# Kernel optimization log

Hardware: AMD Instinct MI355X
Metric: run time of the kernel (lower is better)

The kernel has to match this reference:

```python
import jax, jax.numpy as jnp
import numpy as np

N, E, H, R = 20000, 400000, 128, 20


def setup_inputs() -> dict:
    key = jax.random.key(0)
    ks = jax.random.split(key, 12)
    inv_h = 1.0 / np.sqrt(H)
    inv_r = 1.0 / np.sqrt(R)
    return {
        "s": jax.random.normal(ks[0], (N, H), jnp.float32),
        "v": jax.random.normal(ks[1], (N, 3, H), jnp.float32),
        "edge_rbf": jax.random.normal(ks[2], (E, R), jnp.float32),
        "edge_cutoff": jax.random.uniform(ks[3], (E,), jnp.float32),
        "edge_vec": jax.random.normal(ks[4], (E, 3), jnp.float32),
        "W1": jax.random.normal(ks[5], (H, H), jnp.float32) * inv_h,
        "b1": jnp.zeros((H,), jnp.float32),
        "W2": jax.random.normal(ks[6], (H, 3 * H), jnp.float32) * inv_h,
        "b2": jnp.zeros((3 * H,), jnp.float32),
        "Wr": jax.random.normal(ks[7], (R, 3 * H), jnp.float32) * inv_r,
        "br": jnp.zeros((3 * H,), jnp.float32),
        "edge_index": jax.random.randint(ks[8], (2, E), 0, N, jnp.int64),
    }


def reference(s, v, edge_rbf, edge_cutoff, edge_vec, W1, b1, W2, b2, Wr, br, edge_index):
    i, j = edge_index[0], edge_index[1]
    n = s.shape[0]
    # rbf projection modulated by cutoff: [E, 3H]
    W = (edge_rbf @ Wr + br) * edge_cutoff[:, None]
    # scalar MLP on gathered source features: [E, 3H]
    h = jax.nn.silu(s[j] @ W1 + b1)
    x = (h @ W2 + b2) * W
    x_ss, x_sv, x_vv = jnp.split(x, 3, axis=-1)  # each [E, H]
    ds = jax.ops.segment_sum(x_ss, i, num_segments=n)
    # dv1: outer product of edge direction with gated scalars -> [E,3,H]
    dv1 = jax.ops.segment_sum(x_sv[:, None, :] * edge_vec[:, :, None], i, num_segments=n)
    # equivariant term: project v_j onto edge direction, re-expand
    inner = jnp.sum(v[j] * edge_vec[:, :, None], axis=1)  # [E, H]
    dv2 = jax.ops.segment_sum((inner * x_vv)[:, None, :] * edge_vec[:, :, None], i, num_segments=n)
    return ds, dv1 + dv2
```

## Files before the change

### kernel.cpp

```cpp
#include <hip/hip_runtime.h>
#include <hip/hip_bf16.h>

#define HDIM 128
#define H3   384
#define RDIM 20
#define NPB  16
#define EPB  64

typedef unsigned short u16;
typedef unsigned int   u32;

__device__ __forceinline__ u16 f2bf(float f) {
    __hip_bfloat16 h = __float2bfloat16(f);
    return *(u16*)&h;
}
__device__ __forceinline__ float bflo(u32 u) {
    union { u32 i; float f; } x; x.i = u << 16; return x.f;
}
__device__ __forceinline__ float bfhi(u32 u) {
    union { u32 i; float f; } x; x.i = u & 0xffff0000u; return x.f;
}
__device__ __forceinline__ u32 pk(float lo, float hi) {
    return (u32)f2bf(lo) | ((u32)f2bf(hi) << 16);
}

__global__ __launch_bounds__(128) void node_mlp_kernel(
    const float* __restrict__ s, const float* __restrict__ W1,
    const float* __restrict__ b1, const float* __restrict__ W2,
    const float* __restrict__ b2, const float* __restrict__ v,
    u32* __restrict__ P3, int N)
{
    __shared__ float sS[NPB][HDIM];
    __shared__ float sH[NPB][HDIM];
    const int t  = threadIdx.x;
    const int n0 = blockIdx.x * NPB;

    #pragma unroll
    for (int n = 0; n < NPB; ++n) {
        int node = n0 + n;
        sS[n][t] = (node < N) ? s[(size_t)node * HDIM + t] : 0.f;
    }
    __syncthreads();

    float acc[NPB];
    #pragma unroll
    for (int n = 0; n < NPB; ++n) acc[n] = 0.f;
    for (int k = 0; k < HDIM; ++k) {
        float w = W1[k * HDIM + t];
        #pragma unroll
        for (int n = 0; n < NPB; ++n) acc[n] += sS[n][k] * w;
    }
    float bb = b1[t];
    #pragma unroll
    for (int n = 0; n < NPB; ++n) {
        float z = acc[n] + bb;
        sH[n][t] = z / (1.f + __expf(-z));
    }
    __syncthreads();

    float a0[NPB], a1[NPB], a2[NPB];
    #pragma unroll
    for (int n = 0; n < NPB; ++n) { a0[n] = 0.f; a1[n] = 0.f; a2[n] = 0.f; }
    for (int k2 = 0; k2 < HDIM / 2; ++k2) {
        float2 hv[NPB];
        #pragma unroll
        for (int n = 0; n < NPB; ++n) hv[n] = ((const float2*)sH[n])[k2];
        #pragma unroll
        for (int kk = 0; kk < 2; ++kk) {
            int k = 2 * k2 + kk;
            float w0 = W2[k * H3 + t];
            float w1 = W2[k * H3 + t + 128];
            float w2 = W2[k * H3 + t + 256];
            #pragma unroll
            for (int n = 0; n < NPB; ++n) {
                float h = kk ? hv[n].y : hv[n].x;
                a0[n] += h * w0;
                a1[n] += h * w1;
                a2[n] += h * w2;
            }
        }
    }
    float c0 = b2[t], c1 = b2[t + 128], c2 = b2[t + 256];
    #pragma unroll
    for (int n = 0; n < NPB; ++n) {
        int node = n0 + n;
        if (node < N) {
            size_t vb = (size_t)node * H3;
            float vx = v[vb + t], vy = v[vb + 128 + t], vz = v[vb + 256 + t];
            size_t pb = (size_t)node * H3 + t;
            P3[pb]       = pk(a0[n] + c0, a1[n] + c1);
            P3[pb + 128] = pk(a2[n] + c2, vx);
            P3[pb + 256] = pk(vy, vz);
        }
    }
}

__global__ void hist_kernel(const int* __restrict__ eidx, int* __restrict__ counts, int E)
{
    int e = blockIdx.x * 256 + threadIdx.x;
    if (e < E) atomicAdd(&counts[eidx[e]], 1);
}

__global__ __launch_bounds__(1024) void scan_kernel(
    const int* __restrict__ counts, int* __restrict__ rstart,
    int* __restrict__ cursor, int N)
{
    __shared__ int part[1024];
    const int t = threadIdx.x;
    const int C = 20;
    int loc[C];
    int s = 0;
    #pragma unroll
    for (int q = 0; q < C; ++q) {
        int idx = t * C + q;
        int c = (idx < N) ? counts[idx] : 0;
        loc[q] = s; s += c;
    }
    part[t] = s;
    __syncthreads();
    for (int off = 1; off < 1024; off <<= 1) {
        int vv = (t >= off) ? part[t - off] : 0;
        __syncthreads();
        part[t] += vv;
        __syncthreads();
    }
    int boff = (t > 0) ? part[t - 1] : 0;
    #pragma unroll
    for (int q = 0; q < C; ++q) {
        int idx = t * C + q;
        if (idx < N) {
            int st = boff + loc[q];
            rstart[idx] = st;
            cursor[idx] = st;
        }
    }
    if (t == 1023) rstart[N] = part[1023];
}

__global__ void scatter_kernel(const int* __restrict__ eidx, int* __restrict__ cursor,
                               int* __restrict__ eord, int E)
{
    int e = blockIdx.x * 256 + threadIdx.x;
    if (e < E) {
        int i = eidx[e];
        int pos = atomicAdd(&cursor[i], 1);
        eord[pos] = e;
    }
}

__global__ __launch_bounds__(128, 4) void edge_stream_kernel(
    const int* __restrict__ eord, const int* __restrict__ eidx,
    const float* __restrict__ rbf, const float* __restrict__ cutoff,
    const float* __restrict__ evec, const float* __restrict__ Wr,
    const float* __restrict__ br, const u32* __restrict__ P3,
    float* __restrict__ ds, float* __restrict__ dv, int E)
{
    const int t    = threadIdx.x;
    const int base = blockIdx.x * EPB;
    const int cnt  = min(EPB, E - base);

    float wr[3 * RDIM];
    #pragma unroll
    for (int k = 0; k < RDIM; ++k) {
        wr[k]            = Wr[k * H3 + t];
        wr[RDIM + k]     = Wr[k * H3 + t + 128];
        wr[2 * RDIM + k] = Wr[k * H3 + t + 256];
    }
    float br0 = br[t], br1 = br[t + 128], br2 = br[t + 256];
    #pragma unroll
    for (int k = 0; k < 3 * RDIM; ++k) asm volatile("" : "+v"(wr[k]));
    asm volatile("" : "+v"(br0), "+v"(br1), "+v"(br2));

    __shared__ int   sI[EPB], sJ[EPB];
    __shared__ float sCut[EPB], sVx[EPB], sVy[EPB], sVz[EPB];
    __shared__ __attribute__((aligned(16))) float sRbf[EPB][RDIM];

    if (t < cnt) {
        int e   = eord[base + t];
        sI[t]   = eidx[e];
        sJ[t]   = eidx[E + e] * H3;
        sCut[t] = cutoff[e];
        sVx[t]  = evec[3 * e];
        sVy[t]  = evec[3 * e + 1];
        sVz[t]  = evec[3 * e + 2];
        const float4* rr = (const float4*)(rbf + (size_t)e * RDIM);
        float4* dst = (float4*)sRbf[t];
        #pragma unroll
        for (int j = 0; j < 5; ++j) dst[j] = rr[j];
    }
    __syncthreads();

    u32 ca, cb, cc;
    {
        int idx = sJ[0] + t;
        ca = P3[idx]; cb = P3[idx + 128]; cc = P3[idx + 256];
    }
    int   cur  = sI[0];
    float accs = 0.f, accx = 0.f, accy = 0.f, accz = 0.f;

    for (int q = 0; q < cnt; ++q) {
        u32 na = 0, nb = 0, nc = 0;
        if (q + 1 < cnt) {
            int idx = sJ[q + 1] + t;
            na = P3[idx]; nb = P3[idx + 128]; nc = P3[idx + 256];
        }
        int iq = sI[q];
        if (iq != cur) {
            atomicAdd(&ds[(size_t)cur * HDIM + t], accs);
            size_t dvi = (size_t)cur * H3;
            atomicAdd(&dv[dvi + t],       accx);
            atomicAdd(&dv[dvi + 128 + t], accy);
            atomicAdd(&dv[dvi + 256 + t], accz);
            accs = accx = accy = accz = 0.f;
            cur = iq;
        }
        const float4* r4 = (const float4*)sRbf[q];
        float w0 = 0.f, w1 = 0.f, w2 = 0.f;
        #pragma unroll
        for (int k4 = 0; k4 < 5; ++k4) {
            float4 r = r4[k4];
            w0 += r.x * wr[4*k4]          + r.y * wr[4*k4+1]          + r.z * wr[4*k4+2]          + r.w * wr[4*k4+3];
            w1 += r.x * wr[RDIM+4*k4]     + r.y * wr[RDIM+4*k4+1]     + r.z * wr[RDIM+4*k4+2]     + r.w * wr[RDIM+4*k4+3];
            w2 += r.x * wr[2*RDIM+4*k4]   + r.y * wr[2*RDIM+4*k4+1]   + r.z * wr[2*RDIM+4*k4+2]   + r.w * wr[2*RDIM+4*k4+3];
        }
        float cu = sCut[q];
        float ex = sVx[q], ey = sVy[q], ez = sVz[q];
        float pss = bflo(ca), psv = bfhi(ca);
        float pvv = bflo(cb), vx  = bfhi(cb);
        float vy  = bflo(cc), vz  = bfhi(cc);
        float xss = (w0 + br0) * cu * pss;
        float xsv = (w1 + br1) * cu * psv;
        float xvv = (w2 + br2) * cu * pvv;
        float inner = vx * ex + vy * ey + vz * ez;
        float coef  = xsv + inner * xvv;
        accs += xss;
        accx += coef * ex;
        accy += coef * ey;
        accz += coef * ez;
        ca = na; cb = nb; cc = nc;
    }
    atomicAdd(&ds[(size_t)cur * HDIM + t], accs);
    size_t dvi = (size_t)cur * H3;
    atomicAdd(&dv[dvi + t],       accx);
    atomicAdd(&dv[dvi + 128 + t], accy);
    atomicAdd(&dv[dvi + 256 + t], accz);
}

extern "C" void kernel_launch(void* const* d_in, const int* in_sizes, int n_in,
                              void* d_out, int out_size, void* d_ws, size_t ws_size,
                              hipStream_t stream)
{
    const float* s    = (const float*)d_in[0];
    const float* v    = (const float*)d_in[1];
    const float* rbf  = (const float*)d_in[2];
    const float* cut  = (const float*)d_in[3];
    const float* evec = (const float*)d_in[4];
    const float* W1   = (const float*)d_in[5];
    const float* b1   = (const float*)d_in[6];
    const float* W2   = (const float*)d_in[7];
    const float* b2   = (const float*)d_in[8];
    const float* Wr   = (const float*)d_in[9];
    const float* br   = (const float*)d_in[10];
    const int*   eidx = (const int*)d_in[11];

    const int N = in_sizes[0] / HDIM;
    const int E = in_sizes[3];

    float* out = (float*)d_out;
    float* ds  = out;
    float* dv  = out + (size_t)N * HDIM;

    char* w = (char*)d_ws;
    u32* P3 = (u32*)w;                     w += ((size_t)N * H3 * 4 + 255) / 256 * 256;
    int* counts = (int*)w;                 w += ((size_t)N * 4 + 255) / 256 * 256;
    int* rstart = (int*)w;                 w += ((size_t)(N + 1) * 4 + 255) / 256 * 256;
    int* cursor = (int*)w;                 w += ((size_t)N * 4 + 255) / 256 * 256;
    int* eord   = (int*)w;

    hipMemsetAsync(d_out, 0, (size_t)out_size * sizeof(float), stream);
    hipMemsetAsync(counts, 0, (size_t)N * sizeof(int), stream);

    node_mlp_kernel<<<(N + NPB - 1) / NPB, 128, 0, stream>>>(s, W1, b1, W2, b2, v, P3, N);
    hist_kernel<<<(E + 255) / 256, 256, 0, stream>>>(eidx, counts, E);
    scan_kernel<<<1, 1024, 0, stream>>>(counts, rstart, cursor, N);
    scatter_kernel<<<(E + 255) / 256, 256, 0, stream>>>(eidx, cursor, eord, E);
    edge_stream_kernel<<<(E + EPB - 1) / EPB, 128, 0, stream>>>(eord, eidx, rbf, cut,
                                                                evec, Wr, br, P3,
                                                                ds, dv, E);
}
```

Before: 318.6 us.

## Split edge kernel into three warp-role groups per output component

The edge streaming kernel now runs 384 threads per block, split into three 128-thread roles that handle the ss, sv and vv channels separately, each with its own 20-weight register slice. Per-thread register pressure drops from 60 weights and 4 accumulators. The rbf rows are no longer staged in shared memory; each role streams them straight from global memory with a one-edge-ahead prefetch. Edges per block double to 128. In exchange, each rbf row is read three times and dv gets two atomic contributions per element (roles 1 and 2) instead of one, which raises atomic traffic.

```diff
diff --git a/kernel.cpp b/kernel.cpp
--- a/kernel.cpp
+++ b/kernel.cpp
@@ -5,7 +5,8 @@
 #define H3   384
 #define RDIM 20
 #define NPB  16
-#define EPB  64
+#define EPB  128
+#define TPB  384
 
 typedef unsigned short u16;
 typedef unsigned int   u32;
@@ -148,7 +149,18 @@
     }
 }
 
-__global__ __launch_bounds__(128, 4) void edge_stream_kernel(
+#define LOAD_ROW(dst, q) {                                           \
+    const float4* rp = (const float4*)(rbf + (size_t)sE[q] * RDIM);  \
+    dst[0]=rp[0]; dst[1]=rp[1]; dst[2]=rp[2]; dst[3]=rp[3]; dst[4]=rp[4]; }
+
+#define DOT20(res, rr) {                                                         \
+    res = brv;                                                                   \
+    _Pragma("unroll")                                                            \
+    for (int k4 = 0; k4 < 5; ++k4)                                               \
+        res += rr[k4].x*wr[4*k4] + rr[k4].y*wr[4*k4+1] +                         \
+               rr[k4].z*wr[4*k4+2] + rr[k4].w*wr[4*k4+3]; }
+
+__global__ __launch_bounds__(TPB) void edge_stream_kernel(
     const int* __restrict__ eord, const int* __restrict__ eidx,
     const float* __restrict__ rbf, const float* __restrict__ cutoff,
     const float* __restrict__ evec, const float* __restrict__ Wr,
@@ -156,94 +168,126 @@
     float* __restrict__ ds, float* __restrict__ dv, int E)
 {
     const int t    = threadIdx.x;
+    const int ch   = t & (HDIM - 1);
+    const int role = t >> 7;
     const int base = blockIdx.x * EPB;
     const int cnt  = min(EPB, E - base);
 
-    float wr[3 * RDIM];
-    #pragma unroll
-    for (int k = 0; k < RDIM; ++k) {
-        wr[k]            = Wr[k * H3 + t];
-        wr[RDIM + k]     = Wr[k * H3 + t + 128];
-        wr[2 * RDIM + k] = Wr[k * H3 + t + 256];
-    }
-    float br0 = br[t], br1 = br[t + 128], br2 = br[t + 256];
-    #pragma unroll
-    for (int k = 0; k < 3 * RDIM; ++k) asm volatile("" : "+v"(wr[k]));
-    asm volatile("" : "+v"(br0), "+v"(br1), "+v"(br2));
-
-    __shared__ int   sI[EPB], sJ[EPB];
+    float wr[RDIM];
+    #pragma unroll
+    for (int k = 0; k < RDIM; ++k) wr[k] = Wr[k * H3 + role * HDIM + ch];
+    const float brv = br[role * HDIM + ch];
+
+    __shared__ int   sE[EPB], sI[EPB], sJ[EPB];
     __shared__ float sCut[EPB], sVx[EPB], sVy[EPB], sVz[EPB];
-    __shared__ __attribute__((aligned(16))) float sRbf[EPB][RDIM];
 
     if (t < cnt) {
         int e   = eord[base + t];
+        sE[t]   = e;
         sI[t]   = eidx[e];
         sJ[t]   = eidx[E + e] * H3;
         sCut[t] = cutoff[e];
         sVx[t]  = evec[3 * e];
         sVy[t]  = evec[3 * e + 1];
         sVz[t]  = evec[3 * e + 2];
-        const float4* rr = (const float4*)(rbf + (size_t)e * RDIM);
-        float4* dst = (float4*)sRbf[t];
-        #pragma unroll
-        for (int j = 0; j < 5; ++j) dst[j] = rr[j];
     }
     __syncthreads();
 
-    u32 ca, cb, cc;
-    {
-        int idx = sJ[0] + t;
-        ca = P3[idx]; cb = P3[idx + 128]; cc = P3[idx + 256];
-    }
-    int   cur  = sI[0];
-    float accs = 0.f, accx = 0.f, accy = 0.f, accz = 0.f;
-
-    for (int q = 0; q < cnt; ++q) {
-        u32 na = 0, nb = 0, nc = 0;
-        if (q + 1 < cnt) {
-            int idx = sJ[q + 1] + t;
-            na = P3[idx]; nb = P3[idx + 128]; nc = P3[idx + 256];
-        }
-        int iq = sI[q];
-        if (iq != cur) {
-            atomicAdd(&ds[(size_t)cur * HDIM + t], accs);
-            size_t dvi = (size_t)cur * H3;
-            atomicAdd(&dv[dvi + t],       accx);
-            atomicAdd(&dv[dvi + 128 + t], accy);
-            atomicAdd(&dv[dvi + 256 + t], accz);
-            accs = accx = accy = accz = 0.f;
-            cur = iq;
-        }
-        const float4* r4 = (const float4*)sRbf[q];
-        float w0 = 0.f, w1 = 0.f, w2 = 0.f;
-        #pragma unroll
-        for (int k4 = 0; k4 < 5; ++k4) {
-            float4 r = r4[k4];
-            w0 += r.x * wr[4*k4]          + r.y * wr[4*k4+1]          + r.z * wr[4*k4+2]          + r.w * wr[4*k4+3];
-            w1 += r.x * wr[RDIM+4*k4]     + r.y * wr[RDIM+4*k4+1]     + r.z * wr[RDIM+4*k4+2]     + r.w * wr[RDIM+4*k4+3];
-            w2 += r.x * wr[2*RDIM+4*k4]   + r.y * wr[2*RDIM+4*k4+1]   + r.z * wr[2*RDIM+4*k4+2]   + r.w * wr[2*RDIM+4*k4+3];
-        }
-        float cu = sCut[q];
-        float ex = sVx[q], ey = sVy[q], ez = sVz[q];
-        float pss = bflo(ca), psv = bfhi(ca);
-        float pvv = bflo(cb), vx  = bfhi(cb);
-        float vy  = bflo(cc), vz  = bfhi(cc);
-        float xss = (w0 + br0) * cu * pss;
-        float xsv = (w1 + br1) * cu * psv;
-        float xvv = (w2 + br2) * cu * pvv;
-        float inner = vx * ex + vy * ey + vz * ez;
-        float coef  = xsv + inner * xvv;
-        accs += xss;
-        accx += coef * ex;
-        accy += coef * ey;
-        accz += coef * ez;
-        ca = na; cb = nb; cc = nc;
-    }
-    atomicAdd(&ds[(size_t)cur * HDIM + t], accs);
-    size_t dvi = (size_t)cur * H3;
-    atomicAdd(&dv[dvi + t],       accx);
-    atomicAdd(&dv[dvi + 128 + t], accy);
-    atomicAdd(&dv[dvi + 256 + t], accz);
+    int cur = sI[0];
+
+    if (role == 0) {
+        float4 rc[5], rn[5];
+        LOAD_ROW(rc, 0);
+        #pragma unroll
+        for (int j = 0; j < 5; ++j) rn[j] = rc[j];
+        u32 ca = P3[sJ[0] + ch];
+        float accs = 0.f;
+        for (int q = 0; q < cnt; ++q) {
+            int qn = q + 1;
+            u32 na = 0;
+            if (qn < cnt) { LOAD_ROW(rn, qn); na = P3[sJ[qn] + ch]; }
+            if (sI[q] != cur) {
+                atomicAdd(&ds[(size_t)cur * HDIM + ch], accs);
+                accs = 0.f; cur = sI[q];
+            }
+            float w; DOT20(w, rc);
+            accs += w * sCut[q] * bflo(ca);
+            #pragma unroll
+            for (int j = 0; j < 5; ++j) rc[j] = rn[j];
+            ca = na;
+        }
+        atomicAdd(&ds[(size_t)cur * HDIM + ch], accs);
+    } else if (role == 1) {
+        float4 rc[5], rn[5];
+        LOAD_ROW(rc, 0);
+        #pragma unroll
+        for (int j = 0; j < 5; ++j) rn[j] = rc[j];
+        u32 ca = P3[sJ[0] + ch];
+        float ax = 0.f, ay = 0.f, az = 0.f;
+        for (int q = 0; q < cnt; ++q) {
+            int qn = q + 1;
+            u32 na = 0;
+            if (qn < cnt) { LOAD_ROW(rn, qn); na = P3[sJ[qn] + ch]; }
+            if (sI[q] != cur) {
+                size_t dvi = (size_t)cur * H3;
+                atomicAdd(&dv[dvi + ch],       ax);
+                atomicAdd(&dv[dvi + 128 + ch], ay);
+                atomicAdd(&dv[dvi + 256 + ch], az);
+                ax = ay = az = 0.f; cur = sI[q];
+            }
+            float w; DOT20(w, rc);
+            float xsv = w * sCut[q] * bfhi(ca);
+            ax += xsv * sVx[q];
+            ay += xsv * sVy[q];
+            az += xsv * sVz[q];
+            #pragma unroll
+            for (int j = 0; j < 5; ++j) rc[j] = rn[j];
+            ca = na;
+        }
+        size_t dvi = (size_t)cur * H3;
+        atomicAdd(&dv[dvi + ch],       ax);
+        atomicAdd(&dv[dvi + 128 + ch], ay);
+        atomicAdd(&dv[dvi + 256 + ch], az);
+    } else {
+        float4 rc[5], rn[5];
+        LOAD_ROW(rc, 0);
+        #pragma unroll
+        for (int j = 0; j < 5; ++j) rn[j] = rc[j];
+        u32 cb = P3[sJ[0] + 128 + ch];
+        u32 cc = P3[sJ[0] + 256 + ch];
+        float ax = 0.f, ay = 0.f, az = 0.f;
+        for (int q = 0; q < cnt; ++q) {
+            int qn = q + 1;
+            u32 nb = 0, nc = 0;
+            if (qn < cnt) {
+                LOAD_ROW(rn, qn);
+                nb = P3[sJ[qn] + 128 + ch];
+                nc = P3[sJ[qn] + 256 + ch];
+            }
+            if (sI[q] != cur) {
+                size_t dvi = (size_t)cur * H3;
+                atomicAdd(&dv[dvi + ch],       ax);
+                atomicAdd(&dv[dvi + 128 + ch], ay);
+                atomicAdd(&dv[dvi + 256 + ch], az);
+                ax = ay = az = 0.f; cur = sI[q];
+            }
+            float w; DOT20(w, rc);
+            float ex = sVx[q], ey = sVy[q], ez = sVz[q];
+            float xvv   = w * sCut[q] * bflo(cb);
+            float inner = bfhi(cb) * ex + bflo(cc) * ey + bfhi(cc) * ez;
+            float tt    = inner * xvv;
+            ax += tt * ex;
+            ay += tt * ey;
+            az += tt * ez;
+            #pragma unroll
+            for (int j = 0; j < 5; ++j) rc[j] = rn[j];
+            cb = nb; cc = nc;
+        }
+        size_t dvi = (size_t)cur * H3;
+        atomicAdd(&dv[dvi + ch],       ax);
+        atomicAdd(&dv[dvi + 128 + ch], ay);
+        atomicAdd(&dv[dvi + 256 + ch], az);
+    }
 }
 
 extern "C" void kernel_launch(void* const* d_in, const int* in_sizes, int n_in,
@@ -284,7 +328,7 @@
     hist_kernel<<<(E + 255) / 256, 256, 0, stream>>>(eidx, counts, E);
     scan_kernel<<<1, 1024, 0, stream>>>(counts, rstart, cursor, N);
     scatter_kernel<<<(E + 255) / 256, 256, 0, stream>>>(eidx, cursor, eord, E);
-    edge_stream_kernel<<<(E + EPB - 1) / EPB, 128, 0, stream>>>(eord, eidx, rbf, cut,
+    edge_stream_kernel<<<(E + EPB - 1) / EPB, TPB, 0, stream>>>(eord, eidx, rbf, cut,
                                                                 evec, Wr, br, P3,
                                                                 ds, dv, E);
 }
```

Measured after the change: 495.2 us. +55.4%, slower.

## Precompute edge RBF projection with MFMA into bf16 workspace before edge pass

Applied to the files above, without the earlier changes.

Adds a separate kernel that computes the per-edge RBF projection (rbf @ Wr + br) * cutoff with bf16 MFMA instructions and writes it as a bf16 [E,384] buffer in sorted edge order. The edge streaming kernel then reads these precomputed weights instead of doing the 20-wide dot products per edge in FP32 registers, and it processes 128 edges per block. The aim is to move the FP32 ALU work onto matrix cores and free registers for occupancy. In exchange it adds about 300 MB of extra global write and read traffic plus bf16 rounding of the weights, and it keeps the old kernel as a fallback when the workspace is too small.

```diff
diff --git a/kernel.cpp b/kernel.cpp
--- a/kernel.cpp
+++ b/kernel.cpp
@@ -5,14 +5,19 @@
 #define H3   384
 #define RDIM 20
 #define NPB  16
-#define EPB  64
+#define EPB  128
 
 typedef unsigned short u16;
 typedef unsigned int   u32;
+typedef __attribute__((ext_vector_type(8))) short short8v;
+typedef __attribute__((ext_vector_type(4))) float f32x4;
 
 __device__ __forceinline__ u16 f2bf(float f) {
     __hip_bfloat16 h = __float2bfloat16(f);
     return *(u16*)&h;
+}
+__device__ __forceinline__ float bf2f(u16 u) {
+    union { u32 i; float f; } x; x.i = (u32)u << 16; return x.f;
 }
 __device__ __forceinline__ float bflo(u32 u) {
     union { u32 i; float f; } x; x.i = u << 16; return x.f;
@@ -148,7 +153,159 @@
     }
 }
 
-__global__ __launch_bounds__(128, 4) void edge_stream_kernel(
+__global__ __launch_bounds__(256) void wgemm_kernel(
+    const int* __restrict__ eord, const float* __restrict__ rbf,
+    const float* __restrict__ cutoff, const float* __restrict__ Wr,
+    const float* __restrict__ br, u16* __restrict__ Ws, int E)
+{
+    const int lane    = threadIdx.x & 63;
+    const int wave    = threadIdx.x >> 6;
+    const int g       = lane >> 4;
+    const int m       = lane & 15;
+    const int colhalf = wave & 1;
+    const int wgrp    = wave >> 1;
+
+    short8v bfrag[12];
+    float   brt[12];
+    #pragma unroll
+    for (int n = 0; n < 12; ++n) {
+        int col = colhalf * 192 + n * 16 + m;
+        short8v f;
+        #pragma unroll
+        for (int j = 0; j < 8; ++j) {
+            int k = 8 * g + j;
+            f[j] = (k < RDIM) ? (short)f2bf(Wr[k * H3 + col]) : (short)0;
+        }
+        bfrag[n] = f;
+        brt[n] = br[col];
+    }
+
+    const int PBI = 256;
+    for (int it = 0; it < PBI / 32; ++it) {
+        int pbase = blockIdx.x * PBI + it * 32 + wgrp * 16;
+        if (pbase >= E) break;
+
+        short8v af;
+        int posA = pbase + m;
+        if (posA < E && g < 3) {
+            const float* rr = rbf + (size_t)eord[posA] * RDIM;
+            if (g < 2) {
+                float4 r0 = *(const float4*)(rr + 8 * g);
+                float4 r1 = *(const float4*)(rr + 8 * g + 4);
+                af[0] = (short)f2bf(r0.x); af[1] = (short)f2bf(r0.y);
+                af[2] = (short)f2bf(r0.z); af[3] = (short)f2bf(r0.w);
+                af[4] = (short)f2bf(r1.x); af[5] = (short)f2bf(r1.y);
+                af[6] = (short)f2bf(r1.z); af[7] = (short)f2bf(r1.w);
+            } else {
+                float4 r0 = *(const float4*)(rr + 16);
+                af[0] = (short)f2bf(r0.x); af[1] = (short)f2bf(r0.y);
+                af[2] = (short)f2bf(r0.z); af[3] = (short)f2bf(r0.w);
+                af[4] = 0; af[5] = 0; af[6] = 0; af[7] = 0;
+            }
+        } else {
+            #pragma unroll
+            for (int j = 0; j < 8; ++j) af[j] = 0;
+        }
+
+        float cut[4];
+        #pragma unroll
+        for (int r = 0; r < 4; ++r) {
+            int pos = pbase + 4 * g + r;
+            cut[r] = (pos < E) ? cutoff[eord[pos]] : 0.f;
+        }
+
+        #pragma unroll
+        for (int n = 0; n < 12; ++n) {
+            f32x4 c = {0.f, 0.f, 0.f, 0.f};
+            c = __builtin_amdgcn_mfma_f32_16x16x32_bf16(af, bfrag[n], c, 0, 0, 0);
+            int col = colhalf * 192 + n * 16 + m;
+            #pragma unroll
+            for (int r = 0; r < 4; ++r) {
+                int pos = pbase + 4 * g + r;
+                if (pos < E)
+                    Ws[(size_t)pos * H3 + col] = f2bf((c[r] + brt[n]) * cut[r]);
+            }
+        }
+    }
+}
+
+__global__ __launch_bounds__(128) void edge_kernel(
+    const int* __restrict__ eord, const int* __restrict__ eidx,
+    const float* __restrict__ evec, const u16* __restrict__ Ws,
+    const u32* __restrict__ P3, float* __restrict__ ds,
+    float* __restrict__ dv, int E)
+{
+    const int t    = threadIdx.x;
+    const int base = blockIdx.x * EPB;
+    const int cnt  = min(EPB, E - base);
+
+    __shared__ int   sI[EPB], sJ[EPB];
+    __shared__ float sVx[EPB], sVy[EPB], sVz[EPB];
+
+    if (t < cnt) {
+        int e  = eord[base + t];
+        sI[t]  = eidx[e];
+        sJ[t]  = eidx[E + e] * H3;
+        sVx[t] = evec[3 * e];
+        sVy[t] = evec[3 * e + 1];
+        sVz[t] = evec[3 * e + 2];
+    }
+    __syncthreads();
+
+    const u16* wp = Ws + (size_t)base * H3 + t;
+
+    int   cur  = sI[0];
+    float accs = 0.f, accx = 0.f, accy = 0.f, accz = 0.f;
+
+    u32 ca, cb, cc; u16 w0c, w1c, w2c;
+    {
+        int idx = sJ[0] + t;
+        ca = P3[idx]; cb = P3[idx + 128]; cc = P3[idx + 256];
+        w0c = wp[0]; w1c = wp[128]; w2c = wp[256];
+    }
+
+    for (int q = 0; q < cnt; ++q) {
+        u32 na = 0, nb = 0, nc = 0; u16 w0n = 0, w1n = 0, w2n = 0;
+        if (q + 1 < cnt) {
+            int idx = sJ[q + 1] + t;
+            na = P3[idx]; nb = P3[idx + 128]; nc = P3[idx + 256];
+            const u16* wq = wp + (size_t)(q + 1) * H3;
+            w0n = wq[0]; w1n = wq[128]; w2n = wq[256];
+        }
+        if (sI[q] != cur) {
+            atomicAdd(&ds[(size_t)cur * HDIM + t], accs);
+            size_t dvi = (size_t)cur * H3;
+            atomicAdd(&dv[dvi + t],       accx);
+            atomicAdd(&dv[dvi + 128 + t], accy);
+            atomicAdd(&dv[dvi + 256 + t], accz);
+            accs = accx = accy = accz = 0.f;
+            cur = sI[q];
+        }
+        float w0 = bf2f(w0c), w1 = bf2f(w1c), w2 = bf2f(w2c);
+        float ex = sVx[q], ey = sVy[q], ez = sVz[q];
+        float pss = bflo(ca), psv = bfhi(ca);
+        float pvv = bflo(cb), vx  = bfhi(cb);
+        float vy  = bflo(cc), vz  = bfhi(cc);
+        float xss = w0 * pss;
+        float xsv = w1 * psv;
+        float xvv = w2 * pvv;
+        float inner = vx * ex + vy * ey + vz * ez;
+        float coef  = xsv + inner * xvv;
+        accs += xss;
+        accx += coef * ex;
+        accy += coef * ey;
+        accz += coef * ez;
+        ca = na; cb = nb; cc = nc;
+        w0c = w0n; w1c = w1n; w2c = w2n;
+    }
+    atomicAdd(&ds[(size_t)cur * HDIM + t], accs);
+    size_t dvi = (size_t)cur * H3;
+    atomicAdd(&dv[dvi + t],       accx);
+    atomicAdd(&dv[dvi + 128 + t], accy);
+    atomicAdd(&dv[dvi + 256 + t], accz);
+}
+
+__global__ __launch_bounds__(128, 4) void edge_stream_fallback(
     const int* __restrict__ eord, const int* __restrict__ eidx,
     const float* __restrict__ rbf, const float* __restrict__ cutoff,
     const float* __restrict__ evec, const float* __restrict__ Wr,
@@ -156,8 +313,8 @@
     float* __restrict__ ds, float* __restrict__ dv, int E)
 {
     const int t    = threadIdx.x;
-    const int base = blockIdx.x * EPB;
-    const int cnt  = min(EPB, E - base);
+    const int base = blockIdx.x * 64;
+    const int cnt  = min(64, E - base);
 
     float wr[3 * RDIM];
     #pragma unroll
@@ -166,14 +323,11 @@
         wr[RDIM + k]     = Wr[k * H3 + t + 128];
         wr[2 * RDIM + k] = Wr[k * H3 + t + 256];
     }
-    float br0 = br[t], br1 = br[t + 128], br2 = br[t + 256];
-    #pragma unroll
-    for (int k = 0; k < 3 * RDIM; ++k) asm volatile("" : "+v"(wr[k]));
-    asm volatile("" : "+v"(br0), "+v"(br1), "+v"(br2));
-
-    __shared__ int   sI[EPB], sJ[EPB];
-    __shared__ float sCut[EPB], sVx[EPB], sVy[EPB], sVz[EPB];
-    __shared__ __attribute__((aligned(16))) float sRbf[EPB][RDIM];
+    const float br0 = br[t], br1 = br[t + 128], br2 = br[t + 256];
+
+    __shared__ int   sI[64], sJ[64];
+    __shared__ float sCut[64], sVx[64], sVy[64], sVz[64];
+    __shared__ __attribute__((aligned(16))) float sRbf[64][RDIM];
 
     if (t < cnt) {
         int e   = eord[base + t];
@@ -204,24 +358,23 @@
             int idx = sJ[q + 1] + t;
             na = P3[idx]; nb = P3[idx + 128]; nc = P3[idx + 256];
         }
-        int iq = sI[q];
-        if (iq != cur) {
+        if (sI[q] != cur) {
             atomicAdd(&ds[(size_t)cur * HDIM + t], accs);
             size_t dvi = (size_t)cur * H3;
             atomicAdd(&dv[dvi + t],       accx);
             atomicAdd(&dv[dvi + 128 + t], accy);
             atomicAdd(&dv[dvi + 256 + t], accz);
             accs = accx = accy = accz = 0.f;
-            cur = iq;
+            cur = sI[q];
         }
         const float4* r4 = (const float4*)sRbf[q];
         float w0 = 0.f, w1 = 0.f, w2 = 0.f;
         #pragma unroll
         for (int k4 = 0; k4 < 5; ++k4) {
             float4 r = r4[k4];
-            w0 += r.x * wr[4*k4]          + r.y * wr[4*k4+1]          + r.z * wr[4*k4+2]          + r.w * wr[4*k4+3];
-            w1 += r.x * wr[RDIM+4*k4]     + r.y * wr[RDIM+4*k4+1]     + r.z * wr[RDIM+4*k4+2]     + r.w * wr[RDIM+4*k4+3];
-            w2 += r.x * wr[2*RDIM+4*k4]   + r.y * wr[2*RDIM+4*k4+1]   + r.z * wr[2*RDIM+4*k4+2]   + r.w * wr[2*RDIM+4*k4+3];
+            w0 += r.x*wr[4*k4]        + r.y*wr[4*k4+1]        + r.z*wr[4*k4+2]        + r.w*wr[4*k4+3];
+            w1 += r.x*wr[RDIM+4*k4]   + r.y*wr[RDIM+4*k4+1]   + r.z*wr[RDIM+4*k4+2]   + r.w*wr[RDIM+4*k4+3];
+            w2 += r.x*wr[2*RDIM+4*k4] + r.y*wr[2*RDIM+4*k4+1] + r.z*wr[2*RDIM+4*k4+2] + r.w*wr[2*RDIM+4*k4+3];
         }
         float cu = sCut[q];
         float ex = sVx[q], ey = sVy[q], ez = sVz[q];
@@ -270,12 +423,15 @@
     float* ds  = out;
     float* dv  = out + (size_t)N * HDIM;
 
-    char* w = (char*)d_ws;
+    char* w0 = (char*)d_ws;
+    char* w  = w0;
     u32* P3 = (u32*)w;                     w += ((size_t)N * H3 * 4 + 255) / 256 * 256;
     int* counts = (int*)w;                 w += ((size_t)N * 4 + 255) / 256 * 256;
     int* rstart = (int*)w;                 w += ((size_t)(N + 1) * 4 + 255) / 256 * 256;
     int* cursor = (int*)w;                 w += ((size_t)N * 4 + 255) / 256 * 256;
-    int* eord   = (int*)w;
+    int* eord   = (int*)w;                 w += ((size_t)E * 4 + 255) / 256 * 256;
+    u16* Ws     = (u16*)w;                 w += (size_t)E * H3 * 2;
+    bool haveWs = ((size_t)(w - w0) <= ws_size);
 
     hipMemsetAsync(d_out, 0, (size_t)out_size * sizeof(float), stream);
     hipMemsetAsync(counts, 0, (size_t)N * sizeof(int), stream);
@@ -284,7 +440,14 @@
     hist_kernel<<<(E + 255) / 256, 256, 0, stream>>>(eidx, counts, E);
     scan_kernel<<<1, 1024, 0, stream>>>(counts, rstart, cursor, N);
     scatter_kernel<<<(E + 255) / 256, 256, 0, stream>>>(eidx, cursor, eord, E);
-    edge_stream_kernel<<<(E + EPB - 1) / EPB, 128, 0, stream>>>(eord, eidx, rbf, cut,
+
+    if (haveWs) {
+        wgemm_kernel<<<(E + 255) / 256, 256, 0, stream>>>(eord, rbf, cut, Wr, br, Ws, E);
+        edge_kernel<<<(E + EPB - 1) / EPB, 128, 0, stream>>>(eord, eidx, evec, Ws, P3,
+                                                             ds, dv, E);
+    } else {
+        edge_stream_fallback<<<(E + 63) / 64, 128, 0, stream>>>(eord, eidx, rbf, cut,
                                                                 evec, Wr, br, P3,
                                                                 ds, dv, E);
-}
+    }
+}
```

Measured after the change: 319.8 us. Within noise of the previous version (+0.4%).

## Batch edge gathers in groups of eight and stream Wr from cache

Applied to the files above, without the earlier changes.

The edge loop now processes edges in groups of 8. It first issues all 24 packed-feature gathers for the group, then computes the rbf projection for all 8 edges together, reloading Wr rows from global memory (cache) instead of pinning 60 weights in registers. The aim is more memory-level parallelism than the previous one-edge-ahead prefetch, while keeping register pressure bounded by dropping the launch-bounds occupancy hint. The cost is repeated Wr loads per group and possibly lower occupancy, since the occupancy constraint was removed.

```diff
diff --git a/kernel.cpp b/kernel.cpp
--- a/kernel.cpp
+++ b/kernel.cpp
@@ -6,6 +6,7 @@
 #define RDIM 20
 #define NPB  16
 #define EPB  64
+#define GRP  8
 
 typedef unsigned short u16;
 typedef unsigned int   u32;
@@ -148,7 +149,7 @@
     }
 }
 
-__global__ __launch_bounds__(128, 4) void edge_stream_kernel(
+__global__ __launch_bounds__(128) void edge_stream_kernel(
     const int* __restrict__ eord, const int* __restrict__ eidx,
     const float* __restrict__ rbf, const float* __restrict__ cutoff,
     const float* __restrict__ evec, const float* __restrict__ Wr,
@@ -159,17 +160,8 @@
     const int base = blockIdx.x * EPB;
     const int cnt  = min(EPB, E - base);
 
-    float wr[3 * RDIM];
-    #pragma unroll
-    for (int k = 0; k < RDIM; ++k) {
-        wr[k]            = Wr[k * H3 + t];
-        wr[RDIM + k]     = Wr[k * H3 + t + 128];
-        wr[2 * RDIM + k] = Wr[k * H3 + t + 256];
-    }
-    float br0 = br[t], br1 = br[t + 128], br2 = br[t + 256];
-    #pragma unroll
-    for (int k = 0; k < 3 * RDIM; ++k) asm volatile("" : "+v"(wr[k]));
-    asm volatile("" : "+v"(br0), "+v"(br1), "+v"(br2));
+    const float* wp = Wr + t;
+    const float br0 = br[t], br1 = br[t + 128], br2 = br[t + 256];
 
     __shared__ int   sI[EPB], sJ[EPB];
     __shared__ float sCut[EPB], sVx[EPB], sVy[EPB], sVz[EPB];
@@ -190,54 +182,64 @@
     }
     __syncthreads();
 
-    u32 ca, cb, cc;
-    {
-        int idx = sJ[0] + t;
-        ca = P3[idx]; cb = P3[idx + 128]; cc = P3[idx + 256];
-    }
     int   cur  = sI[0];
     float accs = 0.f, accx = 0.f, accy = 0.f, accz = 0.f;
 
-    for (int q = 0; q < cnt; ++q) {
-        u32 na = 0, nb = 0, nc = 0;
-        if (q + 1 < cnt) {
-            int idx = sJ[q + 1] + t;
-            na = P3[idx]; nb = P3[idx + 128]; nc = P3[idx + 256];
-        }
-        int iq = sI[q];
-        if (iq != cur) {
-            atomicAdd(&ds[(size_t)cur * HDIM + t], accs);
-            size_t dvi = (size_t)cur * H3;
-            atomicAdd(&dv[dvi + t],       accx);
-            atomicAdd(&dv[dvi + 128 + t], accy);
-            atomicAdd(&dv[dvi + 256 + t], accz);
-            accs = accx = accy = accz = 0.f;
-            cur = iq;
-        }
-        const float4* r4 = (const float4*)sRbf[q];
-        float w0 = 0.f, w1 = 0.f, w2 = 0.f;
-        #pragma unroll
-        for (int k4 = 0; k4 < 5; ++k4) {
-            float4 r = r4[k4];
-            w0 += r.x * wr[4*k4]          + r.y * wr[4*k4+1]          + r.z * wr[4*k4+2]          + r.w * wr[4*k4+3];
-            w1 += r.x * wr[RDIM+4*k4]     + r.y * wr[RDIM+4*k4+1]     + r.z * wr[RDIM+4*k4+2]     + r.w * wr[RDIM+4*k4+3];
-            w2 += r.x * wr[2*RDIM+4*k4]   + r.y * wr[2*RDIM+4*k4+1]   + r.z * wr[2*RDIM+4*k4+2]   + r.w * wr[2*RDIM+4*k4+3];
-        }
-        float cu = sCut[q];
-        float ex = sVx[q], ey = sVy[q], ez = sVz[q];
-        float pss = bflo(ca), psv = bfhi(ca);
-        float pvv = bflo(cb), vx  = bfhi(cb);
-        float vy  = bflo(cc), vz  = bfhi(cc);
-        float xss = (w0 + br0) * cu * pss;
-        float xsv = (w1 + br1) * cu * psv;
-        float xvv = (w2 + br2) * cu * pvv;
-        float inner = vx * ex + vy * ey + vz * ez;
-        float coef  = xsv + inner * xvv;
-        accs += xss;
-        accx += coef * ex;
-        accy += coef * ey;
-        accz += coef * ez;
-        ca = na; cb = nb; cc = nc;
+    for (int g0 = 0; g0 < cnt; g0 += GRP) {
+        u32 pa[GRP], pb[GRP], pc[GRP];
+        #pragma unroll
+        for (int e = 0; e < GRP; ++e) {
+            int q = g0 + e;
+            int idx = sJ[(q < cnt) ? q : (cnt - 1)] + t;
+            pa[e] = P3[idx]; pb[e] = P3[idx + 128]; pc[e] = P3[idx + 256];
+        }
+
+        float d0[GRP], d1[GRP], d2[GRP];
+        #pragma unroll
+        for (int e = 0; e < GRP; ++e) { d0[e] = br0; d1[e] = br1; d2[e] = br2; }
+        #pragma unroll 4
+        for (int k = 0; k < RDIM; ++k) {
+            float w0 = wp[k * H3];
+            float w1 = wp[k * H3 + 128];
+            float w2 = wp[k * H3 + 256];
+            #pragma unroll
+            for (int e = 0; e < GRP; ++e) {
+                float r = sRbf[g0 + e][k];
+                d0[e] += r * w0;
+                d1[e] += r * w1;
+                d2[e] += r * w2;
+            }
+        }
+
+        #pragma unroll
+        for (int e = 0; e < GRP; ++e) {
+            int q = g0 + e;
+            if (q < cnt) {
+                if (sI[q] != cur) {
+                    atomicAdd(&ds[(size_t)cur * HDIM + t], accs);
+                    size_t dvi = (size_t)cur * H3;
+                    atomicAdd(&dv[dvi + t],       accx);
+                    atomicAdd(&dv[dvi + 128 + t], accy);
+                    atomicAdd(&dv[dvi + 256 + t], accz);
+                    accs = accx = accy = accz = 0.f;
+                    cur = sI[q];
+                }
+                float cu = sCut[q];
+                float ex = sVx[q], ey = sVy[q], ez = sVz[q];
+                float pss = bflo(pa[e]), psv = bfhi(pa[e]);
+                float pvv = bflo(pb[e]), vx  = bfhi(pb[e]);
+                float vy  = bflo(pc[e]), vz  = bfhi(pc[e]);
+                float xss = d0[e] * cu * pss;
+                float xsv = d1[e] * cu * psv;
+                float xvv = d2[e] * cu * pvv;
+                float inner = vx * ex + vy * ey + vz * ez;
+                float coef  = xsv + inner * xvv;
+                accs += xss;
+                accx += coef * ex;
+                accy += coef * ey;
+                accz += coef * ez;
+            }
+        }
     }
     atomicAdd(&ds[(size_t)cur * HDIM + t], accs);
     size_t dvi = (size_t)cur * H3;
```

New measurement: 321.6 us, median of 2. About the same (+0.9%).
